# Kernel tuning notes

Measured on AMD Instinct MI355X. Metric: run time of the kernel, lower is better.

## Reference

```python
import jax, jax.numpy as jnp
import numpy as np

SIGMA = 4.0
KSIZE = 2 * int(4.0 * SIGMA + 0.5) + 1  # 33, as in anomalib's GaussianBlur2d
INPUT_SIZE = (224, 224)
NUM_NEIGHBORS = 9


def avg_pool_4_1_1(x):
    # nn.AvgPool2d(kernel_size=4, stride=1, padding=1), count_include_pad=True -> divide by 16
    s = jax.lax.reduce_window(x, 0.0, jax.lax.add, (1, 1, 4, 4), (1, 1, 1, 1),
                              ((0, 0), (0, 0), (1, 1), (1, 1)))
    return s / 16.0


def gaussian_kernel1d(ksize, sigma):
    x = jnp.arange(ksize, dtype=jnp.float32) - (ksize - 1) / 2.0
    g = jnp.exp(-0.5 * (x / sigma) ** 2)
    return g / jnp.sum(g)


def gaussian_blur(x):
    # separable 33x33 gaussian blur, reflect padding (kornia GaussianBlur2d default)
    k = gaussian_kernel1d(KSIZE, SIGMA)
    pad = KSIZE // 2
    xp = jnp.pad(x, ((0, 0), (0, 0), (pad, pad), (pad, pad)), mode='reflect')
    dn = ('NCHW', 'OIHW', 'NCHW')
    y = jax.lax.conv_general_dilated(xp, k.reshape(1, 1, KSIZE, 1), (1, 1), 'VALID', dimension_numbers=dn)
    y = jax.lax.conv_general_dilated(y, k.reshape(1, 1, 1, KSIZE), (1, 1), 'VALID', dimension_numbers=dn)
    return y


def euclidean_dist(x, y):
    # pairwise L2: x [..., n, d], y [..., m, d] -> [..., n, m]
    x2 = jnp.sum(x * x, axis=-1, keepdims=True)
    y2 = jnp.sum(y * y, axis=-1, keepdims=True)
    d2 = x2 - 2.0 * jnp.matmul(x, jnp.swapaxes(y, -1, -2)) + jnp.swapaxes(y2, -1, -2)
    return jnp.sqrt(jnp.clip(d2, 0.0, None))


def compute_anomaly_score(patch_scores, locations, embedding, memory_bank):
    # PatchCore re-weighting (num_neighbors > 1 branch)
    B, P = patch_scores.shape
    bidx = jnp.arange(B)
    max_patches = jnp.argmax(patch_scores, axis=1)                      # [B]
    feats = embedding.reshape(B, P, -1)[bidx, max_patches]              # [B, C]
    score = patch_scores[bidx, max_patches]                             # [B] s*
    nn_index = locations[bidx, max_patches]                             # [B]
    nn_sample = memory_bank[nn_index]                                   # [B, C]
    d_bank = euclidean_dist(nn_sample, memory_bank)                     # [B, M]
    _, support = jax.lax.top_k(-d_bank, NUM_NEIGHBORS)                  # [B, K] smallest
    support_feats = memory_bank[support]                                # [B, K, C]
    distances = euclidean_dist(feats[:, None, :], support_feats)        # [B, 1, K]
    weights = 1.0 - jnp.exp(score) / jnp.sum(jnp.exp(distances[:, 0, :]), axis=-1)
    return weights * score


def setup_inputs() -> dict:
    key = jax.random.key(0)
    k1, k2, k3 = jax.random.split(key, 3)
    feat_layer2 = jax.random.normal(k1, (8, 512, 28, 28), dtype=jnp.float32)
    feat_layer3 = jax.random.normal(k2, (8, 1024, 14, 14), dtype=jnp.float32)
    memory_bank = jax.random.normal(k3, (32000, 1536), dtype=jnp.float32)
    return {"feat_layer2": feat_layer2, "feat_layer3": feat_layer3, "memory_bank": memory_bank}


def reference(feat_layer2, feat_layer3, memory_bank):
    # feature_pooler = AvgPool2d(4,1,1)
    f2 = avg_pool_4_1_1(feat_layer2)   # [B, 512, 27, 27]
    f3 = avg_pool_4_1_1(feat_layer3)   # [B, 1024, 13, 13]
    B, _, H, W = f2.shape
    # generate_embedding: bilinear upsample layer3 to layer2 size, concat channels
    f3u = jax.image.resize(f3, (B, f3.shape[1], H, W), method='bilinear')
    emb = jnp.concatenate([f2, f3u], axis=1)                            # [B, 1536, 27, 27]
    C = emb.shape[1]
    embedding = jnp.transpose(emb, (0, 2, 3, 1)).reshape(-1, C)         # [B*H*W, C]
    # nearest_neighbors with n_neighbors=1 over the coreset memory bank
    d = euclidean_dist(embedding, memory_bank)                          # [B*H*W, M]
    patch_scores = jnp.min(d, axis=1).reshape(B, -1)
    locations = jnp.argmin(d, axis=1).reshape(B, -1)
    pred_score = compute_anomaly_score(patch_scores, locations, embedding, memory_bank)
    # anomaly map: upsample patch scores to input size + gaussian blur
    pmap = patch_scores.reshape(B, 1, H, W)
    amap = jax.image.resize(pmap, (B, 1, INPUT_SIZE[0], INPUT_SIZE[1]), method='bilinear')
    anomaly_map = gaussian_blur(amap)
    return anomaly_map, pred_score
```

## Files before the change

kernel.cpp:

```cpp
#include <hip/hip_runtime.h>
#include <math.h>

#define NB 8
#define C2 512
#define C3 1024
#define HIN2 28
#define HIN3 14
#define HO2 27
#define HO3 13
#define CC 1536
#define NP (NB*HO2*HO2)
#define NM 32000
#define NKNN 9
#define OH 224
#define AMAP_N (NB*OH*OH)

#define BM 256
#define BN 256
#define BK 64
#define KT (CC/BK)
#define MB_CNT ((NP+BM-1)/BM)
#define NB_CNT (NM/BN)
#define NWG (MB_CNT*NB_CNT)

typedef unsigned long long u64;
typedef unsigned int u32;
typedef __attribute__((ext_vector_type(8))) short bf16x8;
typedef __attribute__((ext_vector_type(4))) float f32x4;

struct GW { float w[33]; };

__device__ __forceinline__ float warp_sum(float v){
  #pragma unroll
  for (int off=32; off; off>>=1) v += __shfl_down(v, off);
  return v;
}

__device__ __forceinline__ ushort f2bf(float f){
  u32 u = __float_as_uint(f);
  u32 r = (u + 0x7FFFu + ((u>>16)&1u)) >> 16;
  return (ushort)r;
}
__device__ __forceinline__ float bf2f(ushort b){
  return __uint_as_float(((u32)b)<<16);
}

#define GLDS(g, l) __builtin_amdgcn_global_load_lds((const __attribute__((address_space(1))) void*)(g), (__attribute__((address_space(3))) void*)(l), 16, 0, 0)
#define WAITVM8() asm volatile("s_waitcnt vmcnt(8)" ::: "memory")
#define WAITVM0() asm volatile("s_waitcnt vmcnt(0)" ::: "memory")
#define WAITLGKM0() asm volatile("s_waitcnt lgkmcnt(0)" ::: "memory")
__device__ __forceinline__ void bar_raw(){
  asm volatile("" ::: "memory");
  __builtin_amdgcn_s_barrier();
  asm volatile("" ::: "memory");
}

__global__ void k_avgpool2(const float* __restrict__ in, ushort* __restrict__ embB){
  int t = blockIdx.x*256 + threadIdx.x;
  if (t >= NB*HO2*HO2*C2) return;
  int c = t % C2; int r = t / C2;
  int j = r % HO2; r /= HO2;
  int i = r % HO2; int b = r / HO2;
  const float* plane = in + ((size_t)(b*C2 + c)*HIN2)*HIN2;
  float s = 0.f;
  #pragma unroll
  for (int di=0; di<4; ++di){
    int y = i - 1 + di;
    if ((unsigned)y >= HIN2) continue;
    #pragma unroll
    for (int dj=0; dj<4; ++dj){
      int x = j - 1 + dj;
      if ((unsigned)x < HIN2) s += plane[y*HIN2 + x];
    }
  }
  embB[((size_t)((b*HO2 + i)*HO2 + j))*CC + c] = f2bf(s * (1.f/16.f));
}

__global__ void k_avgpool3(const float* __restrict__ in, float* __restrict__ f3p){
  int t = blockIdx.x*256 + threadIdx.x;
  if (t >= NB*HO3*HO3*C3) return;
  int c = t % C3; int r = t / C3;
  int j = r % HO3; r /= HO3;
  int i = r % HO3; int b = r / HO3;
  const float* plane = in + ((size_t)(b*C3 + c)*HIN3)*HIN3;
  float s = 0.f;
  #pragma unroll
  for (int di=0; di<4; ++di){
    int y = i - 1 + di;
    if ((unsigned)y >= HIN3) continue;
    #pragma unroll
    for (int dj=0; dj<4; ++dj){
      int x = j - 1 + dj;
      if ((unsigned)x < HIN3) s += plane[y*HIN3 + x];
    }
  }
  f3p[((size_t)((b*HO3 + i)*HO3 + j))*C3 + c] = s * (1.f/16.f);
}

__global__ void k_upsample3(const float* __restrict__ f3p, ushort* __restrict__ embB){
  int t = blockIdx.x*256 + threadIdx.x;
  if (t >= NB*HO2*HO2*C3) return;
  int c = t % C3; int r = t / C3;
  int ox = r % HO2; r /= HO2;
  int oy = r % HO2; int b = r / HO2;
  float fy = (oy + 0.5f) * (13.f/27.f) - 0.5f;
  float fx = (ox + 0.5f) * (13.f/27.f) - 0.5f;
  int y0 = (int)floorf(fy); float wy = fy - (float)y0;
  int x0 = (int)floorf(fx); float wx = fx - (float)x0;
  int y0c = min(max(y0,0), HO3-1), y1c = min(max(y0+1,0), HO3-1);
  int x0c = min(max(x0,0), HO3-1), x1c = min(max(x0+1,0), HO3-1);
  const float* base = f3p + (size_t)(b*HO3*HO3)*C3;
  float v00 = base[(size_t)(y0c*HO3 + x0c)*C3 + c];
  float v01 = base[(size_t)(y0c*HO3 + x1c)*C3 + c];
  float v10 = base[(size_t)(y1c*HO3 + x0c)*C3 + c];
  float v11 = base[(size_t)(y1c*HO3 + x1c)*C3 + c];
  float v = (1.f-wy)*((1.f-wx)*v00 + wx*v01) + wy*((1.f-wx)*v10 + wx*v11);
  embB[((size_t)((b*HO2 + oy)*HO2 + ox))*CC + C2 + c] = f2bf(v);
}

__global__ void k_bank_prep(const float* __restrict__ bank, ushort* __restrict__ bankB,
                            float* __restrict__ y2){
  int wave = threadIdx.x >> 6, lane = threadIdx.x & 63;
  int r = blockIdx.x*4 + wave;
  if (r >= NM) return;
  const float4* p = (const float4*)(bank + (size_t)r*CC);
  ushort4* q = (ushort4*)(bankB + (size_t)r*CC);
  float s = 0.f;
  #pragma unroll
  for (int it=0; it<6; ++it){
    float4 v = p[it*64 + lane];
    s += v.x*v.x + v.y*v.y + v.z*v.z + v.w*v.w;
    ushort4 o; o.x = f2bf(v.x); o.y = f2bf(v.y); o.z = f2bf(v.z); o.w = f2bf(v.w);
    q[it*64 + lane] = o;
  }
  s = warp_sum(s);
  if (lane==0) y2[r] = s;
}

__global__ void k_rowsumsq_bf(const ushort* __restrict__ src, float* __restrict__ dst, int rows){
  int wave = threadIdx.x >> 6;
  int lane = threadIdx.x & 63;
  int r = blockIdx.x*4 + wave;
  if (r >= rows) return;
  const uint4* p = (const uint4*)(src + (size_t)r*CC);
  float s = 0.f;
  #pragma unroll
  for (int it=0; it<3; ++it){
    uint4 v = p[it*64 + lane];
    u32 ws_[4] = {v.x, v.y, v.z, v.w};
    #pragma unroll
    for (int q=0;q<4;q++){
      float lo = __uint_as_float(ws_[q]<<16);
      float hi = __uint_as_float(ws_[q]&0xFFFF0000u);
      s += lo*lo + hi*hi;
    }
  }
  s = warp_sum(s);
  if (lane==0) dst[r] = s;
}

__global__ void k_init(u64* __restrict__ packed){
  int t = blockIdx.x*256 + threadIdx.x;
  if (t < NP) packed[t] = ~0ull;
}

__global__ __launch_bounds__(512, 2) void k_distmin_mfma(
    const ushort* __restrict__ A, const ushort* __restrict__ B,
    const float* __restrict__ x2, const float* __restrict__ y2,
    u64* __restrict__ packed)
{
  __shared__ ushort smem[4*BM*BK];
  ushort* A0 = smem;
  ushort* B0 = smem + BM*BK;
  ushort* A1 = smem + 2*BM*BK;
  ushort* B1 = smem + 3*BM*BK;

  const int tid = threadIdx.x;
  const int w   = tid >> 6;
  const int l   = tid & 63;
  const int wr  = w >> 2;
  const int wc  = w & 3;
  const int ccol = l & 15;
  const int cgrp = l >> 4;

  int orig = blockIdx.x;
  const int q8 = NWG/8, r8 = NWG%8;
  int xcd = orig & 7, sidx = orig >> 3;
  int wg = (xcd < r8 ? xcd*(q8+1) : r8*(q8+1) + (xcd-r8)*q8) + sidx;
  const int mb = wg % MB_CNT;
  const int nb = wg / MB_CNT;
  const int m0 = mb * BM;
  const int n0 = nb * BN;

  const int scol = (((l&7) ^ (l>>3)) * 8);
  size_t aOff[4], bOff[4];
  u32 ldsOff[4];
  #pragma unroll
  for (int c=0;c<4;c++){
    int chunk = w*4 + c;
    int row = chunk*8 + (l>>3);
    aOff[c] = (size_t)min(m0 + row, NP-1)*CC + scol;
    bOff[c] = (size_t)(n0 + row)*CC + scol;
    ldsOff[c] = chunk*1024 + l*16;
  }

  const u32 o0 = (u32)((cgrp ^ (ccol & 7)) * 8);
  u32 aRow[8], bRow[4];
  #pragma unroll
  for (int mi=0;mi<8;mi++) aRow[mi] = (u32)(wr*128 + mi*16 + ccol)*BK;
  #pragma unroll
  for (int ni=0;ni<4;ni++) bRow[ni] = (u32)(wc*64 + ni*16 + ccol)*BK;

  f32x4 acc[8][4];
  #pragma unroll
  for (int mi=0;mi<8;mi++)
    #pragma unroll
    for (int ni=0;ni<4;ni++)
      acc[mi][ni] = (f32x4){0.f,0.f,0.f,0.f};

  #pragma unroll
  for (int c=0;c<4;c++){
    GLDS(A + aOff[c], (char*)A0 + ldsOff[c]);
    GLDS(B + bOff[c], (char*)B0 + ldsOff[c]);
  }

  const ushort* curA = A0; const ushort* curB = B0;
  ushort* stA = A1; ushort* stB = B1;

  #pragma unroll 1
  for (int kt=0; kt<KT; ++kt){
    if (kt+1 < KT){
      const u32 kk = (u32)(kt+1)*BK;
      #pragma unroll
      for (int c=0;c<4;c++){
        GLDS(A + aOff[c] + kk, (char*)stA + ldsOff[c]);
        GLDS(B + bOff[c] + kk, (char*)stB + ldsOff[c]);
      }
      WAITVM8();
    } else {
      WAITVM0();
    }
    bar_raw();

    #pragma unroll
    for (int ks=0; ks<2; ++ks){
      const u32 so = o0 ^ (u32)(ks<<5);
      bf16x8 a_[8], b_[4];
      #pragma unroll
      for (int mi=0;mi<8;mi++) a_[mi] = *(const bf16x8*)&curA[aRow[mi] + so];
      #pragma unroll
      for (int ni=0;ni<4;ni++) b_[ni] = *(const bf16x8*)&curB[bRow[ni] + so];
      __builtin_amdgcn_s_setprio(1);
      #pragma unroll
      for (int mi=0;mi<8;mi++)
        #pragma unroll
        for (int ni=0;ni<4;ni++)
          acc[mi][ni] = __builtin_amdgcn_mfma_f32_16x16x32_bf16(a_[mi], b_[ni], acc[mi][ni], 0, 0, 0);
      __builtin_amdgcn_s_setprio(0);
    }
    WAITLGKM0();
    __builtin_amdgcn_sched_barrier(0);
    bar_raw();
    ushort* tA = (ushort*)curA; curA = stA; stA = tA;
    ushort* tB = (ushort*)curB; curB = stB; stB = tB;
  }

  float xv[8][4];
  #pragma unroll
  for (int mi=0;mi<8;mi++)
    #pragma unroll
    for (int r=0;r<4;r++)
      xv[mi][r] = x2[min(m0 + wr*128 + mi*16 + cgrp*4 + r, NP-1)];

  u64 best[8][4];
  #pragma unroll
  for (int mi=0;mi<8;mi++)
    #pragma unroll
    for (int r=0;r<4;r++) best[mi][r] = ~0ull;

  #pragma unroll
  for (int ni=0;ni<4;ni++){
    const int n = n0 + wc*64 + ni*16 + ccol;
    const float yy = y2[n];
    #pragma unroll
    for (int mi=0;mi<8;mi++)
      #pragma unroll
      for (int r=0;r<4;r++){
        float d2 = fmaxf(xv[mi][r] + yy - 2.f*acc[mi][ni][r], 0.f);
        u64 pk = (((u64)__float_as_uint(d2))<<32) | (u32)n;
        if (pk < best[mi][r]) best[mi][r] = pk;
      }
  }

  #pragma unroll
  for (int mi=0;mi<8;mi++)
    #pragma unroll
    for (int r=0;r<4;r++){
      u64 pk = best[mi][r];
      #pragma unroll
      for (int md=1; md<16; md<<=1){
        u64 o = __shfl_xor(pk, md);
        if (o < pk) pk = o;
      }
      const int row = m0 + wr*128 + mi*16 + cgrp*4 + r;
      if (ccol==0 && row < NP) atomicMin(&packed[row], pk);
    }
}

__global__ void k_unpack(const u64* __restrict__ packed, float* __restrict__ patch_d, int* __restrict__ loc){
  int t = blockIdx.x*256 + threadIdx.x;
  if (t < NP){
    u64 v = packed[t];
    patch_d[t] = sqrtf(__uint_as_float((u32)(v>>32)));
    loc[t] = (int)(v & 0xffffffffu);
  }
}

__global__ void k_argmax(const float* __restrict__ patch_d, const int* __restrict__ loc,
                         int* __restrict__ sel_mp, float* __restrict__ sel_score, int* __restrict__ sel_nn){
  int b = blockIdx.x;
  int tid = threadIdx.x;
  __shared__ u64 red[4];
  u64 best = 0;
  for (int p = tid; p < HO2*HO2; p += 256){
    float v = patch_d[b*HO2*HO2 + p];
    u64 pk = (((u64)__float_as_uint(v))<<32) | (u32)(HO2*HO2 - p);
    if (pk > best) best = pk;
  }
  int lane = tid & 63, w = tid >> 6;
  #pragma unroll
  for (int d=32; d; d>>=1){ u64 o = __shfl_down(best, d); if (o > best) best = o; }
  if (lane==0) red[w] = best;
  __syncthreads();
  if (tid==0){
    u64 bb = red[0];
    for (int q=1;q<4;q++) if (red[q] > bb) bb = red[q];
    int p = HO2*HO2 - (int)(bb & 0xffffffffu);
    sel_mp[b] = p;
    sel_score[b] = __uint_as_float((u32)(bb>>32));
    sel_nn[b] = loc[b*HO2*HO2 + p];
  }
}

__device__ __forceinline__ void bf8dec(uint4 v, float* f){
  u32 a[4] = {v.x, v.y, v.z, v.w};
  #pragma unroll
  for (int q=0;q<4;q++){
    f[2*q]   = __uint_as_float(a[q]<<16);
    f[2*q+1] = __uint_as_float(a[q]&0xFFFF0000u);
  }
}

__global__ __launch_bounds__(256) void k_dbank(const ushort* __restrict__ bankB, const float* __restrict__ y2,
    const int* __restrict__ sel_nn, float* __restrict__ d_bank){
  int wave = threadIdx.x >> 6, lane = threadIdx.x & 63;
  int m = blockIdx.x*4 + wave;
  if (m >= NM) return;
  int nn[NB];
  #pragma unroll
  for (int b=0;b<NB;b++) nn[b] = sel_nn[b];
  const uint4* pm = (const uint4*)(bankB + (size_t)m*CC);
  float acc[NB];
  #pragma unroll
  for (int b=0;b<NB;b++) acc[b] = 0.f;
  #pragma unroll
  for (int it=0; it<3; ++it){
    uint4 v = pm[it*64 + lane];
    float vf[8]; bf8dec(v, vf);
    #pragma unroll
    for (int b=0;b<NB;b++){
      uint4 u = ((const uint4*)(bankB + (size_t)nn[b]*CC))[it*64 + lane];
      float uf[8]; bf8dec(u, uf);
      #pragma unroll
      for (int q=0;q<8;q++) acc[b] += vf[q]*uf[q];
    }
  }
  #pragma unroll
  for (int b=0;b<NB;b++){
    float s = warp_sum(acc[b]);
    if (lane==0) d_bank[(size_t)b*NM + m] = fmaxf(y2[nn[b]] + y2[m] - 2.f*s, 0.f);
  }
}

__global__ __launch_bounds__(256) void k_score(const float* __restrict__ d_bank, const float* __restrict__ bank,
    const ushort* __restrict__ embB, const float* __restrict__ x2, const float* __restrict__ y2,
    const int* __restrict__ sel_mp, const float* __restrict__ sel_score, float* __restrict__ out_score){
  int b = blockIdx.x, tid = threadIdx.x;
  __shared__ u64 cand[256*NKNN];
  __shared__ int sel[NKNN];
  __shared__ u64 red[4];
  __shared__ u64 gbest_s;
  __shared__ float fred[4];
  __shared__ float sumexp_s;

  #pragma unroll
  for (int q=0;q<NKNN;q++) cand[tid*NKNN+q] = ~0ull;
  for (int m = tid; m < NM; m += 256){
    float v = d_bank[(size_t)b*NM + m];
    u64 pk = (((u64)__float_as_uint(v))<<32) | (u32)m;
    if (pk < cand[tid*NKNN + NKNN-1]){
      cand[tid*NKNN + NKNN-1] = pk;
      for (int q=NKNN-1; q>0 && cand[tid*NKNN+q] < cand[tid*NKNN+q-1]; --q){
        u64 t = cand[tid*NKNN+q]; cand[tid*NKNN+q] = cand[tid*NKNN+q-1]; cand[tid*NKNN+q-1] = t;
      }
    }
  }
  __syncthreads();
  int lane = tid & 63, w = tid >> 6;
  for (int k=0;k<NKNN;++k){
    u64 mybest = ~0ull;
    #pragma unroll
    for (int q=0;q<NKNN;q++){ u64 v = cand[tid*NKNN+q]; if (v < mybest) mybest = v; }
    u64 rb = mybest;
    #pragma unroll
    for (int d=32; d; d>>=1){ u64 o = __shfl_down(rb, d); if (o < rb) rb = o; }
    if (lane==0) red[w] = rb;
    __syncthreads();
    if (tid==0){
      u64 bb = red[0];
      for (int q=1;q<4;q++) if (red[q] < bb) bb = red[q];
      gbest_s = bb;
      sel[k] = (int)(bb & 0xffffffffu);
    }
    __syncthreads();
    u64 gb = gbest_s;
    #pragma unroll
    for (int q=0;q<NKNN;q++) if (cand[tid*NKNN+q] == gb) cand[tid*NKNN+q] = ~0ull;
    __syncthreads();
  }

  int mp = sel_mp[b];
  const ushort* fv = embB + (size_t)(b*HO2*HO2 + mp)*CC;
  float fx2 = x2[b*HO2*HO2 + mp];
  if (tid==0) sumexp_s = 0.f;
  __syncthreads();
  for (int k=0;k<NKNN;++k){
    const float* sv = bank + (size_t)sel[k]*CC;
    float part = 0.f;
    for (int i = tid; i < CC; i += 256) part += bf2f(fv[i])*sv[i];
    part = warp_sum(part);
    if (lane==0) fred[w] = part;
    __syncthreads();
    if (tid==0){
      float dot = fred[0]+fred[1]+fred[2]+fred[3];
      float d2 = fmaxf(fx2 + y2[sel[k]] - 2.f*dot, 0.f);
      sumexp_s += expf(sqrtf(d2));
    }
    __syncthreads();
  }
  if (tid==0){
    float s = sel_score[b];
    out_score[b] = (1.f - expf(s)/sumexp_s) * s;
  }
}

__global__ void k_amap_bilinear(const float* __restrict__ patch_d, float* __restrict__ amap){
  int t = blockIdx.x*256 + threadIdx.x;
  if (t >= AMAP_N) return;
  int x = t % OH; int r = t / OH;
  int y = r % OH; int b = r / OH;
  float fy = (y + 0.5f) * (27.f/224.f) - 0.5f;
  float fx = (x + 0.5f) * (27.f/224.f) - 0.5f;
  int y0 = (int)floorf(fy); float wy = fy - (float)y0;
  int x0 = (int)floorf(fx); float wx = fx - (float)x0;
  int y0c = min(max(y0,0),HO2-1), y1c = min(max(y0+1,0),HO2-1);
  int x0c = min(max(x0,0),HO2-1), x1c = min(max(x0+1,0),HO2-1);
  const float* p = patch_d + b*HO2*HO2;
  float v = (1.f-wy)*((1.f-wx)*p[y0c*HO2+x0c] + wx*p[y0c*HO2+x1c])
          + wy*((1.f-wx)*p[y1c*HO2+x0c] + wx*p[y1c*HO2+x1c]);
  amap[t] = v;
}

__global__ void k_blur_h(const float* __restrict__ in, float* __restrict__ out, GW gw){
  int t = blockIdx.x*256 + threadIdx.x;
  if (t >= AMAP_N) return;
  int x = t % OH; int rest = t / OH;
  const float* row = in + (size_t)rest*OH;
  float s = 0.f;
  #pragma unroll
  for (int k=0;k<33;++k){
    int xx = x + k - 16;
    xx = (xx < 0) ? -xx : xx;
    xx = (xx > OH-1) ? (2*(OH-1) - xx) : xx;
    s += gw.w[k]*row[xx];
  }
  out[t] = s;
}

__global__ void k_blur_v(const float* __restrict__ in, float* __restrict__ out, GW gw){
  int t = blockIdx.x*256 + threadIdx.x;
  if (t >= AMAP_N) return;
  int x = t % OH; int r = t / OH;
  int y = r % OH; int b = r / OH;
  const float* img = in + (size_t)b*OH*OH;
  float s = 0.f;
  #pragma unroll
  for (int k=0;k<33;++k){
    int yy = y + k - 16;
    yy = (yy < 0) ? -yy : yy;
    yy = (yy > OH-1) ? (2*(OH-1) - yy) : yy;
    s += gw.w[k]*img[(size_t)yy*OH + x];
  }
  out[t] = s;
}

extern "C" void kernel_launch(void* const* d_in, const int* in_sizes, int n_in,
                              void* d_out, int out_size, void* d_ws, size_t ws_size,
                              hipStream_t stream){
  const float* f2   = (const float*)d_in[0];
  const float* f3   = (const float*)d_in[1];
  const float* bank = (const float*)d_in[2];
  float* out = (float*)d_out;

  char* ws = (char*)d_ws;
  size_t off = 0;
  auto alloc = [&](size_t bytes)->char*{ char* p = ws + off; off += (bytes + 255) & ~(size_t)255; return p; };
  ushort* embB    = (ushort*)alloc((size_t)NP*CC*2);
  ushort* bankB   = (ushort*)alloc((size_t)NM*CC*2);
  float* f3p      = (float*)alloc((size_t)NB*HO3*HO3*C3*4);
  float* y2       = (float*)alloc((size_t)NM*4);
  float* x2       = (float*)alloc((size_t)NP*4);
  u64*   packed   = (u64*)  alloc((size_t)NP*8);
  float* patch_d  = (float*)alloc((size_t)NP*4);
  int*   loc      = (int*)  alloc((size_t)NP*4);
  float* d_bank   = (float*)alloc((size_t)NB*NM*4);
  int*   sel_mp   = (int*)  alloc(NB*4);
  float* sel_scr  = (float*)alloc(NB*4);
  int*   sel_nn   = (int*)  alloc(NB*4);
  float* amap1    = (float*)alloc((size_t)AMAP_N*4);
  float* amap2    = (float*)alloc((size_t)AMAP_N*4);

  GW gw;
  { float s=0.f; for(int i=0;i<33;i++){ float xx=(float)i-16.f; gw.w[i]=expf(-0.5f*(xx/4.f)*(xx/4.f)); s+=gw.w[i]; }
    for(int i=0;i<33;i++) gw.w[i]/=s; }

  k_avgpool2<<<(NB*HO2*HO2*C2+255)/256,256,0,stream>>>(f2, embB);
  k_avgpool3<<<(NB*HO3*HO3*C3+255)/256,256,0,stream>>>(f3, f3p);
  k_upsample3<<<(NB*HO2*HO2*C3+255)/256,256,0,stream>>>(f3p, embB);
  k_bank_prep<<<(NM+3)/4,256,0,stream>>>(bank, bankB, y2);
  k_rowsumsq_bf<<<(NP+3)/4,256,0,stream>>>(embB, x2, NP);
  k_init<<<(NP+255)/256,256,0,stream>>>(packed);
  k_distmin_mfma<<<NWG,512,0,stream>>>(embB, bankB, x2, y2, packed);
  k_unpack<<<(NP+255)/256,256,0,stream>>>(packed, patch_d, loc);
  k_argmax<<<NB,256,0,stream>>>(patch_d, loc, sel_mp, sel_scr, sel_nn);
  k_dbank<<<(NM+3)/4,256,0,stream>>>(bankB, y2, sel_nn, d_bank);
  k_score<<<NB,256,0,stream>>>(d_bank, bank, embB, x2, y2, sel_mp, sel_scr, out + AMAP_N);
  k_amap_bilinear<<<(AMAP_N+255)/256,256,0,stream>>>(patch_d, amap1);
  k_blur_h<<<(AMAP_N+255)/256,256,0,stream>>>(amap1, amap2, gw);
  k_blur_v<<<(AMAP_N+255)/256,256,0,stream>>>(amap2, out, gw);
}
```

Baseline: 1.111 ms.

## Split distmin GEMM K-step into four quadrant phases with interleaved LDS prefetch

```diff
diff --git a/kernel.cpp b/kernel.cpp
--- a/kernel.cpp
+++ b/kernel.cpp
@@ -46,9 +46,8 @@
 }
 
 #define GLDS(g, l) __builtin_amdgcn_global_load_lds((const __attribute__((address_space(1))) void*)(g), (__attribute__((address_space(3))) void*)(l), 16, 0, 0)
-#define WAITVM8() asm volatile("s_waitcnt vmcnt(8)" ::: "memory")
+#define WAITVM2() asm volatile("s_waitcnt vmcnt(2)" ::: "memory")
 #define WAITVM0() asm volatile("s_waitcnt vmcnt(0)" ::: "memory")
-#define WAITLGKM0() asm volatile("s_waitcnt lgkmcnt(0)" ::: "memory")
 __device__ __forceinline__ void bar_raw(){
   asm volatile("" ::: "memory");
   __builtin_amdgcn_s_barrier();
@@ -170,10 +169,10 @@
     u64* __restrict__ packed)
 {
   __shared__ ushort smem[4*BM*BK];
-  ushort* A0 = smem;
-  ushort* B0 = smem + BM*BK;
-  ushort* A1 = smem + 2*BM*BK;
-  ushort* B1 = smem + 3*BM*BK;
+  ushort* As0 = smem;
+  ushort* Bs0 = smem + BM*BK;
+  ushort* As1 = smem + 2*BM*BK;
+  ushort* Bs1 = smem + 3*BM*BK;
 
   const int tid = threadIdx.x;
   const int w   = tid >> 6;
@@ -192,16 +191,25 @@
   const int m0 = mb * BM;
   const int n0 = nb * BN;
 
-  const int scol = (((l&7) ^ (l>>3)) * 8);
-  size_t aOff[4], bOff[4];
-  u32 ldsOff[4];
-  #pragma unroll
-  for (int c=0;c<4;c++){
-    int chunk = w*4 + c;
-    int row = chunk*8 + (l>>3);
-    aOff[c] = (size_t)min(m0 + row, NP-1)*CC + scol;
-    bOff[c] = (size_t)(n0 + row)*CC + scol;
-    ldsOff[c] = chunk*1024 + l*16;
+  const int rowin = l >> 3;
+  const int scol  = (((l&7) ^ rowin) * 8);
+  int chA1[2], chA2[2], chB1[2], chB2[2];
+  u32 aO1[2], aO2[2], bO1[2], bO2[2];
+  u32 lA1[2], lA2[2], lB1[2], lB2[2];
+  #pragma unroll
+  for (int c=0;c<2;c++){
+    chA1[c] = (w<4) ? (2*w+c) : (8+2*w+c);
+    chA2[c] = chA1[c] + 8;
+    chB1[c] = (w>>1)*8 + (w&1)*2 + c;
+    chB2[c] = chB1[c] + 4;
+    aO1[c] = (u32)min(m0 + chA1[c]*8 + rowin, NP-1)*CC + scol;
+    aO2[c] = (u32)min(m0 + chA2[c]*8 + rowin, NP-1)*CC + scol;
+    bO1[c] = (u32)(n0 + chB1[c]*8 + rowin)*CC + scol;
+    bO2[c] = (u32)(n0 + chB2[c]*8 + rowin)*CC + scol;
+    lA1[c] = (u32)chA1[c]*1024 + l*16;
+    lA2[c] = (u32)chA2[c]*1024 + l*16;
+    lB1[c] = (u32)chB1[c]*1024 + l*16;
+    lB2[c] = (u32)chB2[c]*1024 + l*16;
   }
 
   const u32 o0 = (u32)((cgrp ^ (ccol & 7)) * 8);
@@ -218,52 +226,111 @@
     for (int ni=0;ni<4;ni++)
       acc[mi][ni] = (f32x4){0.f,0.f,0.f,0.f};
 
-  #pragma unroll
-  for (int c=0;c<4;c++){
-    GLDS(A + aOff[c], (char*)A0 + ldsOff[c]);
-    GLDS(B + bOff[c], (char*)B0 + ldsOff[c]);
-  }
-
-  const ushort* curA = A0; const ushort* curB = B0;
-  ushort* stA = A1; ushort* stB = B1;
+  bf16x8 rAlo[4][2], rAhi[4][2], rBlo[2][2], rBhi[2][2];
+
+  #pragma unroll
+  for (int c=0;c<2;c++) GLDS(A + aO1[c], (char*)As0 + lA1[c]);
+  #pragma unroll
+  for (int c=0;c<2;c++) GLDS(B + bO1[c], (char*)Bs0 + lB1[c]);
+  WAITVM0(); bar_raw();
+  #pragma unroll
+  for (int mi=0;mi<4;mi++)
+    #pragma unroll
+    for (int ks=0;ks<2;ks++)
+      rAlo[mi][ks] = *(const bf16x8*)&As0[aRow[mi] + (o0 ^ (u32)(ks<<5))];
+  #pragma unroll
+  for (int ni=0;ni<2;ni++)
+    #pragma unroll
+    for (int ks=0;ks<2;ks++)
+      rBlo[ni][ks] = *(const bf16x8*)&Bs0[bRow[ni] + (o0 ^ (u32)(ks<<5))];
+  #pragma unroll
+  for (int c=0;c<2;c++) GLDS(B + bO2[c], (char*)Bs0 + lB2[c]);
+  #pragma unroll
+  for (int c=0;c<2;c++) GLDS(A + aO2[c], (char*)As0 + lA2[c]);
+
+  const ushort* cA = As0; const ushort* cB = Bs0;
+  ushort* nA = As1; ushort* nB = Bs1;
 
   #pragma unroll 1
   for (int kt=0; kt<KT; ++kt){
-    if (kt+1 < KT){
-      const u32 kk = (u32)(kt+1)*BK;
-      #pragma unroll
-      for (int c=0;c<4;c++){
-        GLDS(A + aOff[c] + kk, (char*)stA + ldsOff[c]);
-        GLDS(B + bOff[c] + kk, (char*)stB + ldsOff[c]);
-      }
-      WAITVM8();
-    } else {
-      WAITVM0();
-    }
-    bar_raw();
-
-    #pragma unroll
-    for (int ks=0; ks<2; ++ks){
-      const u32 so = o0 ^ (u32)(ks<<5);
-      bf16x8 a_[8], b_[4];
-      #pragma unroll
-      for (int mi=0;mi<8;mi++) a_[mi] = *(const bf16x8*)&curA[aRow[mi] + so];
-      #pragma unroll
-      for (int ni=0;ni<4;ni++) b_[ni] = *(const bf16x8*)&curB[bRow[ni] + so];
-      __builtin_amdgcn_s_setprio(1);
-      #pragma unroll
-      for (int mi=0;mi<8;mi++)
+    const u32 kk = (u32)(kt+1)*BK;
+
+    WAITVM2(); bar_raw(); __builtin_amdgcn_sched_barrier(0);
+    GLDS(A + aO1[0] + kk, (char*)nA + lA1[0]);
+    GLDS(A + aO1[1] + kk, (char*)nA + lA1[1]);
+    #pragma unroll
+    for (int ni=0;ni<2;ni++)
+      #pragma unroll
+      for (int ks=0;ks<2;ks++)
+        rBhi[ni][ks] = *(const bf16x8*)&cB[bRow[ni+2] + (o0 ^ (u32)(ks<<5))];
+    __builtin_amdgcn_s_setprio(1);
+    #pragma unroll
+    for (int mi=0;mi<4;mi++)
+      #pragma unroll
+      for (int ni=0;ni<2;ni++)
         #pragma unroll
-        for (int ni=0;ni<4;ni++)
-          acc[mi][ni] = __builtin_amdgcn_mfma_f32_16x16x32_bf16(a_[mi], b_[ni], acc[mi][ni], 0, 0, 0);
-      __builtin_amdgcn_s_setprio(0);
-    }
-    WAITLGKM0();
-    __builtin_amdgcn_sched_barrier(0);
-    bar_raw();
-    ushort* tA = (ushort*)curA; curA = stA; stA = tA;
-    ushort* tB = (ushort*)curB; curB = stB; stB = tB;
-  }
+        for (int ks=0;ks<2;ks++)
+          acc[mi][ni] = __builtin_amdgcn_mfma_f32_16x16x32_bf16(rAlo[mi][ks], rBlo[ni][ks], acc[mi][ni], 0, 0, 0);
+    __builtin_amdgcn_s_setprio(0);
+
+    WAITVM2(); bar_raw(); __builtin_amdgcn_sched_barrier(0);
+    GLDS(B + bO1[0] + kk, (char*)nB + lB1[0]);
+    GLDS(B + bO1[1] + kk, (char*)nB + lB1[1]);
+    #pragma unroll
+    for (int mi=0;mi<4;mi++)
+      #pragma unroll
+      for (int ks=0;ks<2;ks++)
+        rAhi[mi][ks] = *(const bf16x8*)&cA[aRow[mi+4] + (o0 ^ (u32)(ks<<5))];
+    __builtin_amdgcn_s_setprio(1);
+    #pragma unroll
+    for (int mi=0;mi<4;mi++)
+      #pragma unroll
+      for (int ni=0;ni<2;ni++)
+        #pragma unroll
+        for (int ks=0;ks<2;ks++)
+          acc[mi][ni+2] = __builtin_amdgcn_mfma_f32_16x16x32_bf16(rAlo[mi][ks], rBhi[ni][ks], acc[mi][ni+2], 0, 0, 0);
+    __builtin_amdgcn_s_setprio(0);
+
+    WAITVM2(); bar_raw(); __builtin_amdgcn_sched_barrier(0);
+    GLDS(B + bO2[0] + kk, (char*)nB + lB2[0]);
+    GLDS(B + bO2[1] + kk, (char*)nB + lB2[1]);
+    #pragma unroll
+    for (int mi=0;mi<4;mi++)
+      #pragma unroll
+      for (int ks=0;ks<2;ks++)
+        rAlo[mi][ks] = *(const bf16x8*)&((const ushort*)nA)[aRow[mi] + (o0 ^ (u32)(ks<<5))];
+    __builtin_amdgcn_s_setprio(1);
+    #pragma unroll
+    for (int mi=0;mi<4;mi++)
+      #pragma unroll
+      for (int ni=0;ni<2;ni++)
+        #pragma unroll
+        for (int ks=0;ks<2;ks++)
+          acc[mi+4][ni] = __builtin_amdgcn_mfma_f32_16x16x32_bf16(rAhi[mi][ks], rBlo[ni][ks], acc[mi+4][ni], 0, 0, 0);
+    __builtin_amdgcn_s_setprio(0);
+
+    WAITVM2(); bar_raw(); __builtin_amdgcn_sched_barrier(0);
+    GLDS(A + aO2[0] + kk, (char*)nA + lA2[0]);
+    GLDS(A + aO2[1] + kk, (char*)nA + lA2[1]);
+    #pragma unroll
+    for (int ni=0;ni<2;ni++)
+      #pragma unroll
+      for (int ks=0;ks<2;ks++)
+        rBlo[ni][ks] = *(const bf16x8*)&((const ushort*)nB)[bRow[ni] + (o0 ^ (u32)(ks<<5))];
+    __builtin_amdgcn_s_setprio(1);
+    #pragma unroll
+    for (int mi=0;mi<4;mi++)
+      #pragma unroll
+      for (int ni=0;ni<2;ni++)
+        #pragma unroll
+        for (int ks=0;ks<2;ks++)
+          acc[mi+4][ni+2] = __builtin_amdgcn_mfma_f32_16x16x32_bf16(rAhi[mi][ks], rBhi[ni][ks], acc[mi+4][ni+2], 0, 0, 0);
+    __builtin_amdgcn_s_setprio(0);
+
+    ushort* t1 = (ushort*)cA; cA = nA; nA = t1;
+    ushort* t2 = (ushort*)cB; cB = nB; nB = t2;
+  }
+  WAITVM0();
 
   float xv[8][4];
   #pragma unroll
```

Result: faster. 1.041 ms (-6.3%).
